# Optimization experiments

Hardware: AMD Instinct MI355X
Metric: run time of the kernel (lower is better)

Reference implementation:

```python
import jax, jax.numpy as jnp
import numpy as np

B, T, IN_CH, CODE = 512, 256, 32, 256


def _lstm_cell(x, h, c, wih, whh, bih, bhh):
    # torch gate order: i, f, g, o
    gates = x @ wih.T + bih + h @ whh.T + bhh
    i, f, g, o = jnp.split(gates, 4, axis=-1)
    c_new = jax.nn.sigmoid(f) * c + jax.nn.sigmoid(i) * jnp.tanh(g)
    h_new = jax.nn.sigmoid(o) * jnp.tanh(c_new)
    return h_new, c_new


def setup_inputs() -> dict:
    key = jax.random.key(0)
    ks = jax.random.split(key, 12)
    def xavier(k, shape):
        fan_in, fan_out = shape[1], shape[0]
        lim = float(np.sqrt(6.0 / (fan_in + fan_out)))
        return jax.random.uniform(k, shape, jnp.float32, -lim, lim)
    def uni(k, shape, dim):
        lim = 1.0 / float(np.sqrt(dim))
        return jax.random.uniform(k, shape, jnp.float32, -lim, lim)
    return {
        "x": jax.random.normal(ks[0], (B, T, IN_CH), jnp.float32),
        "w_enc": xavier(ks[1], (CODE, IN_CH)),
        "b_enc": jnp.zeros((CODE,), jnp.float32),
        "wih_e": uni(ks[2], (4 * CODE, CODE), CODE),
        "whh_e": uni(ks[3], (4 * CODE, CODE), CODE),
        "bih_e": uni(ks[4], (4 * CODE,), CODE),
        "bhh_e": uni(ks[5], (4 * CODE,), CODE),
        "wih_d": uni(ks[6], (4 * CODE, CODE), CODE),
        "whh_d": uni(ks[7], (4 * CODE, CODE), CODE),
        "bih_d": uni(ks[8], (4 * CODE,), CODE),
        "bhh_d": uni(ks[9], (4 * CODE,), CODE),
        "w_dec": xavier(ks[10], (IN_CH, CODE)),
        "b_dec": jnp.zeros((IN_CH,), jnp.float32),
    }


def reference(x, w_enc, b_enc, wih_e, whh_e, bih_e, bhh_e,
              wih_d, whh_d, bih_d, bhh_d, w_dec, b_dec):
    batch, window, _ = x.shape
    code = w_enc.shape[0]
    # instance encoder: [B, T, IN] -> [B, T, CODE]
    x_enc = x @ w_enc.T + b_enc

    # temporal encoder LSTM; keep only final (h, c)
    def enc_step(carry, xt):
        h, c = carry
        h, c = _lstm_cell(xt, h, c, wih_e, whh_e, bih_e, bhh_e)
        return (h, c), None
    h0 = jnp.zeros((batch, code), x.dtype)
    (h_T, c_T), _ = jax.lax.scan(enc_step, (h0, h0), jnp.swapaxes(x_enc, 0, 1))
    code_vec = h_T  # [B, CODE]

    # decoder: feed back LSTM output as next input; project each step
    def dec_step(carry, _):
        inp, h, c = carry
        h, c = _lstm_cell(inp, h, c, wih_d, whh_d, bih_d, bhh_d)
        out_t = h @ w_dec.T + b_dec  # [B, IN]
        return (h, h, c), out_t
    init = (jnp.zeros_like(code_vec), h_T, c_T)
    _, outs = jax.lax.scan(dec_step, init, None, length=window)
    out = jnp.swapaxes(outs, 0, 1)  # [B, T, IN]
    return code_vec, out
```

## Files before the change

kernel.cpp:

```cpp
#include <hip/hip_runtime.h>
#include <hip/hip_bf16.h>

#define B_    512
#define T_    256
#define INCH  32
#define C_    256

typedef __bf16 bf16_t;
typedef bf16_t bf16x8 __attribute__((ext_vector_type(8)));
typedef float  f32x4  __attribute__((ext_vector_type(4)));

#define OFF_WHHE 0
#define OFF_WCMB 524288
#define OFF_WHHD 1048576
#define OFF_WIN  1572864
#define OFF_WDEC 1638400
#define OFF_BE   1654784
#define OFF_BD   1658880
#define WS_NEED  1662976

__device__ __forceinline__ float sigf(float x) {
  float e = exp2f(-1.4426950408889634f * x);
  return __builtin_amdgcn_rcpf(1.0f + e);
}
__device__ __forceinline__ float tanh_fast(float x) {
  float e = exp2f(2.8853900817779268f * x);
  return 1.0f - 2.0f * __builtin_amdgcn_rcpf(1.0f + e);
}

__global__ void prep_pack_big(const float* __restrict__ whh_e,
                              const float* __restrict__ wih_d,
                              const float* __restrict__ whh_d,
                              char* __restrict__ ws) {
  int t = blockIdx.x * blockDim.x + threadIdx.x;
  int m   = t >> 15;
  int r   = t & 32767;
  int blk = r >> 6;
  int l   = r & 63;
  int nt  = blk >> 3, kt = blk & 7;
  int g   = nt * 16 + (l & 15);
  int k0  = kt * 32 + (l >> 4) * 8;
  const float* s0; const float* s1 = nullptr; char* dst;
  if (m == 0)      { s0 = whh_e; dst = ws + OFF_WHHE; }
  else if (m == 1) { s0 = wih_d; s1 = whh_d; dst = ws + OFF_WCMB; }
  else             { s0 = whh_d; dst = ws + OFF_WHHD; }
  bf16x8 v;
  #pragma unroll
  for (int i = 0; i < 8; ++i) {
    float a = s0[(size_t)g * C_ + k0 + i];
    if (s1) a += s1[(size_t)g * C_ + k0 + i];
    v[i] = (bf16_t)a;
  }
  *(bf16x8*)(dst + (size_t)blk * 1024 + l * 16) = v;
}

__global__ void prep_small(const float* __restrict__ w_enc,
                           const float* __restrict__ b_enc,
                           const float* __restrict__ wih_e,
                           const float* __restrict__ bih_e,
                           const float* __restrict__ bhh_e,
                           const float* __restrict__ bih_d,
                           const float* __restrict__ bhh_d,
                           const float* __restrict__ w_dec,
                           char* __restrict__ ws) {
  int t = blockIdx.x * blockDim.x + threadIdx.x;
  if (t < 32768) {
    int nt = t >> 9;
    int r  = t & 511;
    int l  = r >> 3;
    int i  = r & 7;
    int g  = nt * 16 + (l & 15);
    int j  = (l >> 4) * 8 + i;
    float s = 0.f;
    for (int c = 0; c < C_; ++c)
      s += wih_e[(size_t)g * C_ + c] * w_enc[(size_t)c * INCH + j];
    ((bf16_t*)(ws + OFF_WIN))[(size_t)nt * 512 + l * 8 + i] = (bf16_t)s;
  } else if (t < 32768 + 8192) {
    int r   = t - 32768;
    int blk = r >> 9;
    int q   = r & 511;
    int l   = q >> 3;
    int i   = q & 7;
    int ntv = blk >> 3, kt = blk & 7;
    int n   = ntv * 16 + (l & 15);
    int k   = kt * 32 + (l >> 4) * 8 + i;
    ((bf16_t*)(ws + OFF_WDEC))[(size_t)blk * 512 + l * 8 + i] =
        (bf16_t)w_dec[(size_t)n * C_ + k];
  } else if (t < 32768 + 8192 + 1024) {
    int g = t - 40960;
    float s = bih_e[g] + bhh_e[g];
    for (int c = 0; c < C_; ++c) s += wih_e[(size_t)g * C_ + c] * b_enc[c];
    ((float*)(ws + OFF_BE))[g] = s;
  } else if (t < 43008) {
    int g = t - 41984;
    ((float*)(ws + OFF_BD))[g] = bih_d[g] + bhh_d[g];
  }
}

__global__ __launch_bounds__(512, 2) void tae_persist(
    const float* __restrict__ x,
    const char*  __restrict__ ws,
    const float* __restrict__ b_dec,
    float* __restrict__ out)
{
  const bf16_t* __restrict__ whhE  = (const bf16_t*)(ws + OFF_WHHE);
  const bf16_t* __restrict__ wCMB  = (const bf16_t*)(ws + OFF_WCMB);
  const bf16_t* __restrict__ whhD  = (const bf16_t*)(ws + OFF_WHHD);
  const bf16_t* __restrict__ winP  = (const bf16_t*)(ws + OFF_WIN);
  const bf16_t* __restrict__ wdecP = (const bf16_t*)(ws + OFF_WDEC);
  const float*  __restrict__ bE    = (const float*)(ws + OFF_BE);
  const float*  __restrict__ bD    = (const float*)(ws + OFF_BD);

  const int b0   = blockIdx.x * 16;
  const int tid  = threadIdx.x;
  const int lane = tid & 63;
  const int wv   = tid >> 6;
  const int fr   = lane & 15;
  const int lg   = lane >> 4;
  const int jt0  = wv * 2;

  __shared__ __align__(16) unsigned char hb[2][8192];
  {
    f32x4 z = {0.f, 0.f, 0.f, 0.f};
    ((f32x4*)hb[0])[tid] = z;
  }
  __syncthreads();

  float creg[2][4];
  #pragma unroll
  for (int a2 = 0; a2 < 2; ++a2)
    #pragma unroll
    for (int q = 0; q < 4; ++q) creg[a2][q] = 0.f;

  float biasE[2][4], biasD[2][4];
  #pragma unroll
  for (int a2 = 0; a2 < 2; ++a2)
    #pragma unroll
    for (int g = 0; g < 4; ++g) {
      biasE[a2][g] = bE[g * C_ + (jt0 + a2) * 16 + fr];
      biasD[a2][g] = bD[g * C_ + (jt0 + a2) * 16 + fr];
    }

  int pb = 0;

  for (int t = 0; t < T_; ++t) {
    bf16x8 ah[8];
    #pragma unroll
    for (int kt = 0; kt < 8; ++kt) {
      int off = fr * 512 + ((kt * 64 + lg * 16) ^ ((fr & 7) << 4));
      ah[kt] = *(const bf16x8*)(hb[pb] + off);
    }
    bf16x8 ax;
    {
      const float* xp = x + (((size_t)(b0 + fr)) * T_ + t) * INCH + lg * 8;
      f32x4 x0 = *(const f32x4*)xp;
      f32x4 x1 = *(const f32x4*)(xp + 4);
      #pragma unroll
      for (int i = 0; i < 4; ++i) { ax[i] = (bf16_t)x0[i]; ax[4 + i] = (bf16_t)x1[i]; }
    }
    f32x4 acc[2][4];
    #pragma unroll
    for (int a2 = 0; a2 < 2; ++a2) {
      #pragma unroll
      for (int g = 0; g < 4; ++g) {
        float bv = biasE[a2][g];
        f32x4 ac = {bv, bv, bv, bv};
        int nt = g * 16 + jt0 + a2;
        ac = __builtin_amdgcn_mfma_f32_16x16x32_bf16(
                 ax, *(const bf16x8*)(winP + (size_t)nt * 512 + lane * 8), ac, 0, 0, 0);
        const bf16_t* bp = whhE + (size_t)nt * 4096 + lane * 8;
        #pragma unroll
        for (int kt = 0; kt < 8; ++kt)
          ac = __builtin_amdgcn_mfma_f32_16x16x32_bf16(
                   ah[kt], *(const bf16x8*)(bp + kt * 512), ac, 0, 0, 0);
        acc[a2][g] = ac;
      }
    }
    const bool last = (t == T_ - 1);
    #pragma unroll
    for (int a2 = 0; a2 < 2; ++a2) {
      #pragma unroll
      for (int q = 0; q < 4; ++q) {
        float iv = sigf(acc[a2][0][q]);
        float fv = sigf(acc[a2][1][q]);
        float gv = tanh_fast(acc[a2][2][q]);
        float ov = sigf(acc[a2][3][q]);
        float cn = fv * creg[a2][q] + iv * gv;
        creg[a2][q] = cn;
        float hn = ov * tanh_fast(cn);
        int rb = lg * 4 + q;
        int j  = (jt0 + a2) * 16 + fr;
        int off = rb * 512 + ((j * 2) ^ ((rb & 7) << 4));
        *(bf16_t*)(hb[pb ^ 1] + off) = (bf16_t)hn;
        if (last) out[(size_t)(b0 + rb) * C_ + j] = hn;
      }
    }
    pb ^= 1;
    __syncthreads();
  }

  const float bdec = (wv < 2) ? b_dec[wv * 16 + fr] : 0.f;
  const size_t SEQ0 = (size_t)B_ * C_;

  for (int t = 0; t < T_; ++t) {
    bf16x8 ah[8];
    #pragma unroll
    for (int kt = 0; kt < 8; ++kt) {
      int off = fr * 512 + ((kt * 64 + lg * 16) ^ ((fr & 7) << 4));
      ah[kt] = *(const bf16x8*)(hb[pb] + off);
    }
    if (wv < 2 && t > 0) {
      f32x4 ay = {bdec, bdec, bdec, bdec};
      const bf16_t* yp = wdecP + (size_t)wv * 4096 + lane * 8;
      #pragma unroll
      for (int kt = 0; kt < 8; ++kt)
        ay = __builtin_amdgcn_mfma_f32_16x16x32_bf16(
                 ah[kt], *(const bf16x8*)(yp + kt * 512), ay, 0, 0, 0);
      #pragma unroll
      for (int q = 0; q < 4; ++q) {
        int rb = lg * 4 + q;
        out[SEQ0 + ((size_t)(b0 + rb) * T_ + (t - 1)) * INCH + wv * 16 + fr] = ay[q];
      }
    }
    const bf16_t* wb = (t == 0) ? whhD : wCMB;
    f32x4 acc[2][4];
    #pragma unroll
    for (int a2 = 0; a2 < 2; ++a2) {
      #pragma unroll
      for (int g = 0; g < 4; ++g) {
        float bv = biasD[a2][g];
        f32x4 ac = {bv, bv, bv, bv};
        int nt = g * 16 + jt0 + a2;
        const bf16_t* bp = wb + (size_t)nt * 4096 + lane * 8;
        #pragma unroll
        for (int kt = 0; kt < 8; ++kt)
          ac = __builtin_amdgcn_mfma_f32_16x16x32_bf16(
                   ah[kt], *(const bf16x8*)(bp + kt * 512), ac, 0, 0, 0);
        acc[a2][g] = ac;
      }
    }
    #pragma unroll
    for (int a2 = 0; a2 < 2; ++a2) {
      #pragma unroll
      for (int q = 0; q < 4; ++q) {
        float iv = sigf(acc[a2][0][q]);
        float fv = sigf(acc[a2][1][q]);
        float gv = tanh_fast(acc[a2][2][q]);
        float ov = sigf(acc[a2][3][q]);
        float cn = fv * creg[a2][q] + iv * gv;
        creg[a2][q] = cn;
        float hn = ov * tanh_fast(cn);
        int rb = lg * 4 + q;
        int j  = (jt0 + a2) * 16 + fr;
        int off = rb * 512 + ((j * 2) ^ ((rb & 7) << 4));
        *(bf16_t*)(hb[pb ^ 1] + off) = (bf16_t)hn;
      }
    }
    pb ^= 1;
    __syncthreads();
  }

  if (wv < 2) {
    bf16x8 ah[8];
    #pragma unroll
    for (int kt = 0; kt < 8; ++kt) {
      int off = fr * 512 + ((kt * 64 + lg * 16) ^ ((fr & 7) << 4));
      ah[kt] = *(const bf16x8*)(hb[pb] + off);
    }
    f32x4 ay = {bdec, bdec, bdec, bdec};
    const bf16_t* yp = wdecP + (size_t)wv * 4096 + lane * 8;
    #pragma unroll
    for (int kt = 0; kt < 8; ++kt)
      ay = __builtin_amdgcn_mfma_f32_16x16x32_bf16(
               ah[kt], *(const bf16x8*)(yp + kt * 512), ay, 0, 0, 0);
    #pragma unroll
    for (int q = 0; q < 4; ++q) {
      int rb = lg * 4 + q;
      out[SEQ0 + ((size_t)(b0 + rb) * T_ + (T_ - 1)) * INCH + wv * 16 + fr] = ay[q];
    }
  }
}

__global__ __launch_bounds__(512) void tae_f32(
    const float* __restrict__ x,
    const float* __restrict__ w_enc, const float* __restrict__ b_enc,
    const float* __restrict__ wih_e, const float* __restrict__ whh_e,
    const float* __restrict__ bih_e, const float* __restrict__ bhh_e,
    const float* __restrict__ wih_d, const float* __restrict__ whh_d,
    const float* __restrict__ bih_d, const float* __restrict__ bhh_d,
    const float* __restrict__ w_dec, const float* __restrict__ b_dec,
    float* __restrict__ out)
{
  const int b0   = blockIdx.x * 4;
  const int tid  = threadIdx.x;
  const int g0   = tid * 2;
  const int type = g0 >> 8;

  __shared__ __align__(16) float hs[2][4][256];
  __shared__ __align__(16) float cs[4][256];
  __shared__ __align__(16) float xe[4][256];
  __shared__ __align__(16) float gsm[4][4][256];

  for (int i = tid; i < 1024; i += 512) { ((float*)hs)[i] = 0.f; ((float*)cs)[i] = 0.f; }
  __syncthreads();

  const float brE[2] = { bih_e[g0] + bhh_e[g0], bih_e[g0 + 1] + bhh_e[g0 + 1] };
  int pb = 0;

  for (int t = 0; t < T_; ++t) {
    #pragma unroll
    for (int u = 0; u < 2; ++u) {
      int item = g0 + u;
      int row = item >> 8, c = item & 255;
      const f32x4* wr = (const f32x4*)(w_enc + (size_t)c * INCH);
      const f32x4* xr = (const f32x4*)(x + ((size_t)(b0 + row) * T_ + t) * INCH);
      f32x4 a = {0.f, 0.f, 0.f, 0.f};
      #pragma unroll
      for (int q = 0; q < 8; ++q) a += wr[q] * xr[q];
      xe[row][c] = b_enc[c] + a[0] + a[1] + a[2] + a[3];
    }
    __syncthreads();
    f32x4 acc[2][4];
    #pragma unroll
    for (int u = 0; u < 2; ++u)
      #pragma unroll
      for (int row = 0; row < 4; ++row) acc[u][row] = (f32x4){0.f,0.f,0.f,0.f};
    for (int k = 0; k < C_; k += 4) {
      f32x4 wx0 = *(const f32x4*)(wih_e + (size_t)g0 * C_ + k);
      f32x4 wx1 = *(const f32x4*)(wih_e + (size_t)(g0 + 1) * C_ + k);
      f32x4 wh0 = *(const f32x4*)(whh_e + (size_t)g0 * C_ + k);
      f32x4 wh1 = *(const f32x4*)(whh_e + (size_t)(g0 + 1) * C_ + k);
      #pragma unroll
      for (int row = 0; row < 4; ++row) {
        f32x4 xv = *(const f32x4*)(&xe[row][k]);
        f32x4 hv = *(const f32x4*)(&hs[pb][row][k]);
        acc[0][row] += wx0 * xv + wh0 * hv;
        acc[1][row] += wx1 * xv + wh1 * hv;
      }
    }
    #pragma unroll
    for (int u = 0; u < 2; ++u)
      #pragma unroll
      for (int row = 0; row < 4; ++row) {
        f32x4 a = acc[u][row];
        gsm[type][row][(g0 + u) & 255] = brE[u] + a[0] + a[1] + a[2] + a[3];
      }
    __syncthreads();
    if (tid < 128) {
      int row = tid >> 5, jb = tid & 31;
      #pragma unroll
      for (int v = 0; v < 8; ++v) {
        int j = jb * 8 + v;
        float iv = 1.f/(1.f+expf(-gsm[0][row][j]));
        float fv = 1.f/(1.f+expf(-gsm[1][row][j]));
        float gv = tanhf(gsm[2][row][j]);
        float ov = 1.f/(1.f+expf(-gsm[3][row][j]));
        float cn = fv*cs[row][j] + iv*gv;
        cs[row][j] = cn;
        float hn = ov*tanhf(cn);
        hs[pb ^ 1][row][j] = hn;
        if (t == T_ - 1) out[(size_t)(b0 + row) * C_ + j] = hn;
      }
    }
    pb ^= 1;
    __syncthreads();
  }

  const float brD[2] = { bih_d[g0] + bhh_d[g0], bih_d[g0 + 1] + bhh_d[g0 + 1] };
  const size_t SEQ0 = (size_t)B_ * C_;

  for (int t = 0; t < T_; ++t) {
    f32x4 acc[2][4];
    #pragma unroll
    for (int u = 0; u < 2; ++u)
      #pragma unroll
      for (int row = 0; row < 4; ++row) acc[u][row] = (f32x4){0.f,0.f,0.f,0.f};
    for (int k = 0; k < C_; k += 4) {
      f32x4 w0 = *(const f32x4*)(whh_d + (size_t)g0 * C_ + k);
      f32x4 w1 = *(const f32x4*)(whh_d + (size_t)(g0 + 1) * C_ + k);
      if (t > 0) {
        w0 += *(const f32x4*)(wih_d + (size_t)g0 * C_ + k);
        w1 += *(const f32x4*)(wih_d + (size_t)(g0 + 1) * C_ + k);
      }
      #pragma unroll
      for (int row = 0; row < 4; ++row) {
        f32x4 hv = *(const f32x4*)(&hs[pb][row][k]);
        acc[0][row] += w0 * hv;
        acc[1][row] += w1 * hv;
      }
    }
    #pragma unroll
    for (int u = 0; u < 2; ++u)
      #pragma unroll
      for (int row = 0; row < 4; ++row) {
        f32x4 a = acc[u][row];
        gsm[type][row][(g0 + u) & 255] = brD[u] + a[0] + a[1] + a[2] + a[3];
      }
    __syncthreads();
    if (tid < 128) {
      int row = tid >> 5, jb = tid & 31;
      #pragma unroll
      for (int v = 0; v < 8; ++v) {
        int j = jb * 8 + v;
        float iv = 1.f/(1.f+expf(-gsm[0][row][j]));
        float fv = 1.f/(1.f+expf(-gsm[1][row][j]));
        float gv = tanhf(gsm[2][row][j]);
        float ov = 1.f/(1.f+expf(-gsm[3][row][j]));
        float cn = fv*cs[row][j] + iv*gv;
        cs[row][j] = cn;
        hs[pb ^ 1][row][j] = ov*tanhf(cn);
      }
    }
    pb ^= 1;
    __syncthreads();
    if (tid < 128) {
      int row = tid >> 5, n = tid & 31;
      const f32x4* wr = (const f32x4*)(w_dec + (size_t)n * C_);
      f32x4 a = {0.f, 0.f, 0.f, 0.f};
      for (int q = 0; q < 64; ++q) a += wr[q] * *(const f32x4*)(&hs[pb][row][q * 4]);
      out[SEQ0 + ((size_t)(b0 + row) * T_ + t) * INCH + n] =
          b_dec[n] + a[0] + a[1] + a[2] + a[3];
    }
  }
}

extern "C" void kernel_launch(void* const* d_in, const int* in_sizes, int n_in,
                              void* d_out, int out_size, void* d_ws, size_t ws_size,
                              hipStream_t stream) {
  const float* x     = (const float*)d_in[0];
  const float* w_enc = (const float*)d_in[1];
  const float* b_enc = (const float*)d_in[2];
  const float* wih_e = (const float*)d_in[3];
  const float* whh_e = (const float*)d_in[4];
  const float* bih_e = (const float*)d_in[5];
  const float* bhh_e = (const float*)d_in[6];
  const float* wih_d = (const float*)d_in[7];
  const float* whh_d = (const float*)d_in[8];
  const float* bih_d = (const float*)d_in[9];
  const float* bhh_d = (const float*)d_in[10];
  const float* w_dec = (const float*)d_in[11];
  const float* b_dec = (const float*)d_in[12];

  if (ws_size >= WS_NEED) {
    char* ws = (char*)d_ws;
    prep_pack_big<<<384, 256, 0, stream>>>(whh_e, wih_d, whh_d, ws);
    prep_small<<<168, 256, 0, stream>>>(w_enc, b_enc, wih_e, bih_e, bhh_e,
                                        bih_d, bhh_d, w_dec, ws);
    tae_persist<<<32, 512, 0, stream>>>(x, ws, b_dec, (float*)d_out);
  } else {
    tae_f32<<<128, 512, 0, stream>>>(x, w_enc, b_enc, wih_e, whh_e, bih_e, bhh_e,
                                     wih_d, whh_d, bih_d, bhh_d, w_dec, b_dec,
                                     (float*)d_out);
  }
}
```

Before: 5.044 ms.

## Software-pipeline recurrent weight loads and keep small weights in registers

```diff
diff --git a/kernel.cpp b/kernel.cpp
--- a/kernel.cpp
+++ b/kernel.cpp
@@ -120,11 +120,6 @@
   const int jt0  = wv * 2;
 
   __shared__ __align__(16) unsigned char hb[2][8192];
-  {
-    f32x4 z = {0.f, 0.f, 0.f, 0.f};
-    ((f32x4*)hb[0])[tid] = z;
-  }
-  __syncthreads();
 
   float creg[2][4];
   #pragma unroll
@@ -141,50 +136,106 @@
       biasD[a2][g] = bD[g * C_ + (jt0 + a2) * 16 + fr];
     }
 
+  bf16x8 winres[8];
+  #pragma unroll
+  for (int p = 0; p < 8; ++p) {
+    const int nt = (p & 3) * 16 + jt0 + (p >> 2);
+    winres[p] = *(const bf16x8*)(winP + (size_t)nt * 512 + lane * 8);
+  }
+
+  bf16x8 wf[4][8];
   int pb = 0;
 
-  for (int t = 0; t < T_; ++t) {
+  {
+    const float* xp = x + ((size_t)(b0 + fr)) * T_ * INCH + lg * 8;
+    f32x4 x0 = *(const f32x4*)xp;
+    f32x4 x1 = *(const f32x4*)(xp + 4);
+    #pragma unroll
+    for (int p = 0; p < 2; ++p) {
+      const int nt = (p & 3) * 16 + jt0 + (p >> 2);
+      const bf16_t* bp_ = whhE + (size_t)nt * 4096 + lane * 8;
+      #pragma unroll
+      for (int kt = 0; kt < 8; ++kt)
+        wf[p][kt] = *(const bf16x8*)(bp_ + kt * 512);
+    }
+    bf16x8 ax;
+    #pragma unroll
+    for (int i = 0; i < 4; ++i) { ax[i] = (bf16_t)x0[i]; ax[4 + i] = (bf16_t)x1[i]; }
+    #pragma unroll
+    for (int a2 = 0; a2 < 2; ++a2) {
+      f32x4 acc[4];
+      #pragma unroll
+      for (int g = 0; g < 4; ++g) {
+        const int p = a2 * 4 + g;
+        float bv = biasE[a2][g];
+        f32x4 ac = {bv, bv, bv, bv};
+        acc[g] = __builtin_amdgcn_mfma_f32_16x16x32_bf16(ax, winres[p], ac, 0, 0, 0);
+      }
+      #pragma unroll
+      for (int q = 0; q < 4; ++q) {
+        float iv = sigf(acc[0][q]);
+        float fv = sigf(acc[1][q]);
+        float gv = tanh_fast(acc[2][q]);
+        float ov = sigf(acc[3][q]);
+        float cn = fv * creg[a2][q] + iv * gv;
+        creg[a2][q] = cn;
+        float hn = ov * tanh_fast(cn);
+        int rb = lg * 4 + q;
+        int j  = (jt0 + a2) * 16 + fr;
+        int off = rb * 512 + ((j * 2) ^ ((rb & 7) << 4));
+        *(bf16_t*)(hb[pb ^ 1] + off) = (bf16_t)hn;
+      }
+    }
+    pb ^= 1;
+    __syncthreads();
+  }
+
+  for (int t = 1; t < T_; ++t) {
+    const float* xp = x + (((size_t)(b0 + fr)) * T_ + t) * INCH + lg * 8;
+    f32x4 x0 = *(const f32x4*)xp;
+    f32x4 x1 = *(const f32x4*)(xp + 4);
     bf16x8 ah[8];
     #pragma unroll
     for (int kt = 0; kt < 8; ++kt) {
       int off = fr * 512 + ((kt * 64 + lg * 16) ^ ((fr & 7) << 4));
       ah[kt] = *(const bf16x8*)(hb[pb] + off);
     }
+    const bool last = (t == T_ - 1);
     bf16x8 ax;
-    {
-      const float* xp = x + (((size_t)(b0 + fr)) * T_ + t) * INCH + lg * 8;
-      f32x4 x0 = *(const f32x4*)xp;
-      f32x4 x1 = *(const f32x4*)(xp + 4);
-      #pragma unroll
-      for (int i = 0; i < 4; ++i) { ax[i] = (bf16_t)x0[i]; ax[4 + i] = (bf16_t)x1[i]; }
-    }
-    f32x4 acc[2][4];
     #pragma unroll
     for (int a2 = 0; a2 < 2; ++a2) {
+      f32x4 acc[4];
       #pragma unroll
       for (int g = 0; g < 4; ++g) {
+        const int p  = a2 * 4 + g;
+        const int pp = (p + 2) & 7;
+        {
+          const int nt = (pp & 3) * 16 + jt0 + (pp >> 2);
+          const bf16_t* bp_ = whhE + (size_t)nt * 4096 + lane * 8;
+          #pragma unroll
+          for (int kt = 0; kt < 8; ++kt)
+            wf[(p + 2) & 3][kt] = *(const bf16x8*)(bp_ + kt * 512);
+        }
         float bv = biasE[a2][g];
         f32x4 ac = {bv, bv, bv, bv};
-        int nt = g * 16 + jt0 + a2;
-        ac = __builtin_amdgcn_mfma_f32_16x16x32_bf16(
-                 ax, *(const bf16x8*)(winP + (size_t)nt * 512 + lane * 8), ac, 0, 0, 0);
-        const bf16_t* bp = whhE + (size_t)nt * 4096 + lane * 8;
         #pragma unroll
         for (int kt = 0; kt < 8; ++kt)
-          ac = __builtin_amdgcn_mfma_f32_16x16x32_bf16(
-                   ah[kt], *(const bf16x8*)(bp + kt * 512), ac, 0, 0, 0);
-        acc[a2][g] = ac;
-      }
-    }
-    const bool last = (t == T_ - 1);
-    #pragma unroll
-    for (int a2 = 0; a2 < 2; ++a2) {
+          ac = __builtin_amdgcn_mfma_f32_16x16x32_bf16(ah[kt], wf[p & 3][kt], ac, 0, 0, 0);
+        acc[g] = ac;
+      }
+      if (a2 == 0) {
+        #pragma unroll
+        for (int i = 0; i < 4; ++i) { ax[i] = (bf16_t)x0[i]; ax[4 + i] = (bf16_t)x1[i]; }
+      }
+      #pragma unroll
+      for (int g = 0; g < 4; ++g)
+        acc[g] = __builtin_amdgcn_mfma_f32_16x16x32_bf16(ax, winres[a2 * 4 + g], acc[g], 0, 0, 0);
       #pragma unroll
       for (int q = 0; q < 4; ++q) {
-        float iv = sigf(acc[a2][0][q]);
-        float fv = sigf(acc[a2][1][q]);
-        float gv = tanh_fast(acc[a2][2][q]);
-        float ov = sigf(acc[a2][3][q]);
+        float iv = sigf(acc[0][q]);
+        float fv = sigf(acc[1][q]);
+        float gv = tanh_fast(acc[2][q]);
+        float ov = sigf(acc[3][q]);
         float cn = fv * creg[a2][q] + iv * gv;
         creg[a2][q] = cn;
         float hn = ov * tanh_fast(cn);
@@ -202,51 +253,49 @@
   const float bdec = (wv < 2) ? b_dec[wv * 16 + fr] : 0.f;
   const size_t SEQ0 = (size_t)B_ * C_;
 
-  for (int t = 0; t < T_; ++t) {
+  bf16x8 wdres[8];
+  if (wv < 2) {
+    const bf16_t* yp = wdecP + (size_t)wv * 4096 + lane * 8;
+    #pragma unroll
+    for (int kt = 0; kt < 8; ++kt) wdres[kt] = *(const bf16x8*)(yp + kt * 512);
+  }
+
+  {
     bf16x8 ah[8];
     #pragma unroll
     for (int kt = 0; kt < 8; ++kt) {
       int off = fr * 512 + ((kt * 64 + lg * 16) ^ ((fr & 7) << 4));
       ah[kt] = *(const bf16x8*)(hb[pb] + off);
     }
-    if (wv < 2 && t > 0) {
-      f32x4 ay = {bdec, bdec, bdec, bdec};
-      const bf16_t* yp = wdecP + (size_t)wv * 4096 + lane * 8;
+    #pragma unroll
+    for (int p = 0; p < 2; ++p) {
+      const int nt = (p & 3) * 16 + jt0 + (p >> 2);
+      const bf16_t* bp_ = wCMB + (size_t)nt * 4096 + lane * 8;
       #pragma unroll
       for (int kt = 0; kt < 8; ++kt)
-        ay = __builtin_amdgcn_mfma_f32_16x16x32_bf16(
-                 ah[kt], *(const bf16x8*)(yp + kt * 512), ay, 0, 0, 0);
-      #pragma unroll
-      for (int q = 0; q < 4; ++q) {
-        int rb = lg * 4 + q;
-        out[SEQ0 + ((size_t)(b0 + rb) * T_ + (t - 1)) * INCH + wv * 16 + fr] = ay[q];
-      }
-    }
-    const bf16_t* wb = (t == 0) ? whhD : wCMB;
-    f32x4 acc[2][4];
+        wf[p][kt] = *(const bf16x8*)(bp_ + kt * 512);
+    }
     #pragma unroll
     for (int a2 = 0; a2 < 2; ++a2) {
+      f32x4 acc[4];
       #pragma unroll
       for (int g = 0; g < 4; ++g) {
+        const int nt = g * 16 + jt0 + a2;
+        const bf16_t* bp_ = whhD + (size_t)nt * 4096 + lane * 8;
         float bv = biasD[a2][g];
         f32x4 ac = {bv, bv, bv, bv};
-        int nt = g * 16 + jt0 + a2;
-        const bf16_t* bp = wb + (size_t)nt * 4096 + lane * 8;
         #pragma unroll
         for (int kt = 0; kt < 8; ++kt)
           ac = __builtin_amdgcn_mfma_f32_16x16x32_bf16(
-                   ah[kt], *(const bf16x8*)(bp + kt * 512), ac, 0, 0, 0);
-        acc[a2][g] = ac;
-      }
-    }
-    #pragma unroll
-    for (int a2 = 0; a2 < 2; ++a2) {
+                   ah[kt], *(const bf16x8*)(bp_ + kt * 512), ac, 0, 0, 0);
+        acc[g] = ac;
+      }
       #pragma unroll
       for (int q = 0; q < 4; ++q) {
-        float iv = sigf(acc[a2][0][q]);
-        float fv = sigf(acc[a2][1][q]);
-        float gv = tanh_fast(acc[a2][2][q]);
-        float ov = sigf(acc[a2][3][q]);
+        float iv = sigf(acc[0][q]);
+        float fv = sigf(acc[1][q]);
+        float gv = tanh_fast(acc[2][q]);
+        float ov = sigf(acc[3][q]);
         float cn = fv * creg[a2][q] + iv * gv;
         creg[a2][q] = cn;
         float hn = ov * tanh_fast(cn);
@@ -260,19 +309,75 @@
     __syncthreads();
   }
 
-  if (wv < 2) {
+  for (int t = 1; t < T_; ++t) {
     bf16x8 ah[8];
     #pragma unroll
     for (int kt = 0; kt < 8; ++kt) {
       int off = fr * 512 + ((kt * 64 + lg * 16) ^ ((fr & 7) << 4));
       ah[kt] = *(const bf16x8*)(hb[pb] + off);
     }
+    if (wv < 2) {
+      f32x4 ay = {bdec, bdec, bdec, bdec};
+      #pragma unroll
+      for (int kt = 0; kt < 8; ++kt)
+        ay = __builtin_amdgcn_mfma_f32_16x16x32_bf16(ah[kt], wdres[kt], ay, 0, 0, 0);
+      #pragma unroll
+      for (int q = 0; q < 4; ++q) {
+        int rb = lg * 4 + q;
+        out[SEQ0 + ((size_t)(b0 + rb) * T_ + (t - 1)) * INCH + wv * 16 + fr] = ay[q];
+      }
+    }
+    #pragma unroll
+    for (int a2 = 0; a2 < 2; ++a2) {
+      f32x4 acc[4];
+      #pragma unroll
+      for (int g = 0; g < 4; ++g) {
+        const int p  = a2 * 4 + g;
+        const int pp = (p + 2) & 7;
+        {
+          const int nt = (pp & 3) * 16 + jt0 + (pp >> 2);
+          const bf16_t* bp_ = wCMB + (size_t)nt * 4096 + lane * 8;
+          #pragma unroll
+          for (int kt = 0; kt < 8; ++kt)
+            wf[(p + 2) & 3][kt] = *(const bf16x8*)(bp_ + kt * 512);
+        }
+        float bv = biasD[a2][g];
+        f32x4 ac = {bv, bv, bv, bv};
+        #pragma unroll
+        for (int kt = 0; kt < 8; ++kt)
+          ac = __builtin_amdgcn_mfma_f32_16x16x32_bf16(ah[kt], wf[p & 3][kt], ac, 0, 0, 0);
+        acc[g] = ac;
+      }
+      #pragma unroll
+      for (int q = 0; q < 4; ++q) {
+        float iv = sigf(acc[0][q]);
+        float fv = sigf(acc[1][q]);
+        float gv = tanh_fast(acc[2][q]);
+        float ov = sigf(acc[3][q]);
+        float cn = fv * creg[a2][q] + iv * gv;
+        creg[a2][q] = cn;
+        float hn = ov * tanh_fast(cn);
+        int rb = lg * 4 + q;
+        int j  = (jt0 + a2) * 16 + fr;
+        int off = rb * 512 + ((j * 2) ^ ((rb & 7) << 4));
+        *(bf16_t*)(hb[pb ^ 1] + off) = (bf16_t)hn;
+      }
+    }
+    pb ^= 1;
+    __syncthreads();
+  }
+
+  if (wv < 2) {
+    bf16x8 ah[8];
+    #pragma unroll
+    for (int kt = 0; kt < 8; ++kt) {
+      int off = fr * 512 + ((kt * 64 + lg * 16) ^ ((fr & 7) << 4));
+      ah[kt] = *(const bf16x8*)(hb[pb] + off);
+    }
     f32x4 ay = {bdec, bdec, bdec, bdec};
-    const bf16_t* yp = wdecP + (size_t)wv * 4096 + lane * 8;
     #pragma unroll
     for (int kt = 0; kt < 8; ++kt)
-      ay = __builtin_amdgcn_mfma_f32_16x16x32_bf16(
-               ah[kt], *(const bf16x8*)(yp + kt * 512), ay, 0, 0, 0);
+      ay = __builtin_amdgcn_mfma_f32_16x16x32_bf16(ah[kt], wdres[kt], ay, 0, 0, 0);
     #pragma unroll
     for (int q = 0; q < 4; ++q) {
       int rb = lg * 4 + q;
```

After: 5.750 ms. 14.0% more time.
